# Kernel optimization log

Measured on AMD Instinct MI355X. Metric: run time of the kernel, lower is better.

The kernel has to match this reference:

```python
import jax, jax.numpy as jnp
import numpy as np

B, F, V, D = 16384, 26, 100000, 64
H1, H2 = 512, 256
IN_DIM = F * D + F * (F - 1) // 2  # 1664 + 325 = 1989
# upper-triangle (i<j) pair indices in row-major order == itertools.combinations order
IU, JU = np.triu_indices(F, k=1)


def setup_inputs() -> dict:
    key = jax.random.key(0)
    ks = jax.random.split(key, 9)
    idx = jax.random.randint(ks[0], (B, F), 0, V)
    tables = jax.random.normal(ks[1], (F, V, D), dtype=jnp.float32) * 0.01
    W1 = jax.random.normal(ks[2], (IN_DIM, H1), dtype=jnp.float32) * (IN_DIM ** -0.5)
    b1 = jnp.zeros((H1,), jnp.float32)
    W2 = jax.random.normal(ks[3], (H1, H2), dtype=jnp.float32) * (H1 ** -0.5)
    b2 = jnp.zeros((H2,), jnp.float32)
    W3 = jax.random.normal(ks[4], (H2, 1), dtype=jnp.float32) * (H2 ** -0.5)
    b3 = jnp.zeros((1,), jnp.float32)
    return {"idx": idx, "tables": tables, "W1": W1, "b1": b1,
            "W2": W2, "b2": b2, "W3": W3, "b3": b3}


def reference(idx, tables, W1, b1, W2, b2, W3, b3):
    # embedding lookup: tables[f, idx[b, f]] -> [B, F, D]
    emb = tables[jnp.arange(F)[None, :], idx]
    # fused dot-interaction: batched Gram matrix + triangular gather
    gram = jnp.einsum('bfd,bgd->bfg', emb, emb)  # [B, F, F]
    inter = gram[:, IU, JU]                      # [B, F*(F-1)/2]
    joint = jnp.concatenate([emb.reshape(B, F * D), inter], axis=1)
    h = jax.nn.relu(joint @ W1 + b1)
    h = jax.nn.relu(h @ W2 + b2)
    return (h @ W3 + b3).squeeze(-1)  # [B] logits
```

## Files before the change

### kernel.cpp

```cpp
#include <hip/hip_runtime.h>

#define B_SZ   16384
#define F_N    26
#define V_N    100000
#define D_N    64
#define H1_N   512
#define H2_N   256
#define IN_DIM 1989
#define KPAD   2048

typedef _Float16 half8_t __attribute__((ext_vector_type(8)));
typedef _Float16 half4_t __attribute__((ext_vector_type(4)));
typedef float    floatx4 __attribute__((ext_vector_type(4)));

#define MFMA16(a, b, c) __builtin_amdgcn_mfma_f32_16x16x32_f16((a), (b), (c), 0, 0, 0)

__device__ __forceinline__ void load_lds16(const void* g, void* l) {
    __builtin_amdgcn_global_load_lds(
        (const __attribute__((address_space(1))) unsigned int*)g,
        (__attribute__((address_space(3))) unsigned int*)l,
        16, 0, 0);
}

__global__ __launch_bounds__(256) void prep_w(const float* __restrict__ W,
                                              _Float16* __restrict__ WT,
                                              int K, int N, int Kpad) {
    int t = blockIdx.x * 256 + threadIdx.x;
    if (t >= N * Kpad) return;
    int n = t / Kpad;
    int k = t - n * Kpad;
    WT[t] = (k < K) ? (_Float16)W[(size_t)k * N + n] : (_Float16)0.f;
}

#define EMB_STRIDE 72
#define EMB_PER_SAMPLE (32 * EMB_STRIDE)

__global__ __launch_bounds__(256) void gather_interact(
        const int* __restrict__ idx,
        const float* __restrict__ tables,
        _Float16* __restrict__ joint) {
    __shared__ __align__(16) _Float16 embh[4 * EMB_PER_SAMPLE];
    __shared__ int sidx[4 * F_N];
    const int tid = threadIdx.x;
    const int b0  = blockIdx.x * 4;

    if (tid < 4 * F_N) sidx[tid] = idx[(size_t)b0 * F_N + tid];

    for (int z = tid; z < 4 * 6 * 16; z += 256) {
        int s = z / 96, rem = z % 96;
        int f = F_N + rem / 16, d4 = (rem % 16) * 4;
        half4_t zz; zz[0] = 0; zz[1] = 0; zz[2] = 0; zz[3] = 0;
        *(half4_t*)(embh + s * EMB_PER_SAMPLE + f * EMB_STRIDE + d4) = zz;
    }
    __syncthreads();

    for (int c = tid; c < 4 * F_N * 16; c += 256) {
        int s = c / 416, rem = c % 416;
        int f = rem >> 4, d4 = (rem & 15) * 4;
        const float4 v = *(const float4*)(tables +
                           ((size_t)f * V_N + sidx[s * F_N + f]) * D_N + d4);
        half4_t h;
        h[0] = (_Float16)v.x; h[1] = (_Float16)v.y;
        h[2] = (_Float16)v.z; h[3] = (_Float16)v.w;
        *(half4_t*)(embh + s * EMB_PER_SAMPLE + f * EMB_STRIDE + d4) = h;
        *(half4_t*)(joint + (size_t)(b0 + s) * KPAD + f * D_N + d4) = h;
    }
    for (int q = tid; q < 4 * (KPAD - IN_DIM); q += 256) {
        int s = q / (KPAD - IN_DIM), p = q % (KPAD - IN_DIM);
        joint[(size_t)(b0 + s) * KPAD + IN_DIM + p] = (_Float16)0.f;
    }
    __syncthreads();

    const int wave = tid >> 6, lane = tid & 63;
    const _Float16* eb = embh + wave * EMB_PER_SAMPLE;
    const int fr = lane & 15;
    const int fk = (lane >> 4) * 8;
    floatx4 a00 = {0.f, 0.f, 0.f, 0.f};
    floatx4 a01 = {0.f, 0.f, 0.f, 0.f};
    floatx4 a11 = {0.f, 0.f, 0.f, 0.f};
    #pragma unroll
    for (int k0 = 0; k0 < 64; k0 += 32) {
        half8_t f0 = *(const half8_t*)(eb + fr * EMB_STRIDE + k0 + fk);
        half8_t f1 = *(const half8_t*)(eb + (16 + fr) * EMB_STRIDE + k0 + fk);
        a00 = MFMA16(f0, f0, a00);
        a01 = MFMA16(f0, f1, a01);
        a11 = MFMA16(f1, f1, a11);
    }
    _Float16* jrow = joint + (size_t)(b0 + wave) * KPAD + F_N * D_N;
    #pragma unroll
    for (int r = 0; r < 4; ++r) {
        int mb = (lane >> 4) * 4 + r;
        {
            int m = mb, n = fr;
            if (m < n) jrow[(m * (51 - m)) / 2 + n - m - 1] = (_Float16)a00[r];
        }
        {
            int m = mb, n = 16 + fr;
            if (n < F_N) jrow[(m * (51 - m)) / 2 + n - m - 1] = (_Float16)a01[r];
        }
        {
            int m = 16 + mb, n = 16 + fr;
            if (m < n && n < F_N) jrow[(m * (51 - m)) / 2 + n - m - 1] = (_Float16)a11[r];
        }
    }
}

__global__ __launch_bounds__(256) void gemm_bt(
        const _Float16* __restrict__ A, int lda,
        const _Float16* __restrict__ Bt, int ldb,
        const float* __restrict__ bias,
        _Float16* __restrict__ C, int ldc,
        int K, int nblocks) {
    __shared__ __align__(16) _Float16 As[128 * 32];
    __shared__ __align__(16) _Float16 Bs[128 * 32];
    const int tid  = threadIdx.x;
    const int wave = tid >> 6;
    const int lane = tid & 63;
    const int bm = blockIdx.x / nblocks;
    const int bn = blockIdx.x % nblocks;
    const int m0 = bm * 128, n0 = bn * 128;

    const int c0 = tid, c1 = tid + 256;
    const _Float16* ag0 = A  + (size_t)(m0 + (c0 >> 2)) * lda + (c0 & 3) * 8;
    const _Float16* ag1 = A  + (size_t)(m0 + (c1 >> 2)) * lda + (c1 & 3) * 8;
    const _Float16* bg0 = Bt + (size_t)(n0 + (c0 >> 2)) * ldb + (c0 & 3) * 8;
    const _Float16* bg1 = Bt + (size_t)(n0 + (c1 >> 2)) * ldb + (c1 & 3) * 8;
    char* asd0 = (char*)As + wave * 1024;
    char* asd1 = (char*)As + 4096 + wave * 1024;
    char* bsd0 = (char*)Bs + wave * 1024;
    char* bsd1 = (char*)Bs + 4096 + wave * 1024;

    floatx4 acc[4][4];
    #pragma unroll
    for (int i = 0; i < 4; ++i)
        #pragma unroll
        for (int j = 0; j < 4; ++j) acc[i][j] = (floatx4){0.f, 0.f, 0.f, 0.f};

    const int wm = (wave >> 1) * 64;
    const int wn = (wave & 1) * 64;
    const int fr = lane & 15;
    const int fk = (lane >> 4) * 8;

    for (int k0 = 0; k0 < K; k0 += 32) {
        load_lds16(ag0 + k0, asd0);
        load_lds16(ag1 + k0, asd1);
        load_lds16(bg0 + k0, bsd0);
        load_lds16(bg1 + k0, bsd1);
        __syncthreads();
        half8_t af[4], bf[4];
        #pragma unroll
        for (int i = 0; i < 4; ++i)
            af[i] = *(const half8_t*)(As + (wm + i * 16 + fr) * 32 + fk);
        #pragma unroll
        for (int j = 0; j < 4; ++j)
            bf[j] = *(const half8_t*)(Bs + (wn + j * 16 + fr) * 32 + fk);
        #pragma unroll
        for (int i = 0; i < 4; ++i)
            #pragma unroll
            for (int j = 0; j < 4; ++j)
                acc[i][j] = MFMA16(af[i], bf[j], acc[i][j]);
        __syncthreads();
    }

    const int colb = n0 + wn + fr;
    const int rowb = m0 + wm + (lane >> 4) * 4;
    #pragma unroll
    for (int j = 0; j < 4; ++j) {
        const int c = colb + j * 16;
        const float bv = bias[c];
        #pragma unroll
        for (int i = 0; i < 4; ++i)
            #pragma unroll
            for (int r = 0; r < 4; ++r) {
                float v = acc[i][j][r] + bv;
                v = fmaxf(v, 0.f);
                C[(size_t)(rowb + i * 16 + r) * ldc + c] = (_Float16)v;
            }
    }
}

__global__ __launch_bounds__(256) void final_gemv(
        const _Float16* __restrict__ h2, const float* __restrict__ W3,
        const float* __restrict__ b3, float* __restrict__ out) {
    const int lane = threadIdx.x & 63;
    const int row  = blockIdx.x * 4 + (threadIdx.x >> 6);
    const float4 w = *(const float4*)(W3 + lane * 4);
    const half4_t h = *(const half4_t*)(h2 + (size_t)row * H2_N + lane * 4);
    float s = (float)h[0] * w.x + (float)h[1] * w.y +
              (float)h[2] * w.z + (float)h[3] * w.w;
    #pragma unroll
    for (int off = 32; off > 0; off >>= 1) s += __shfl_down(s, off, 64);
    if (lane == 0) out[row] = s + b3[0];
}

extern "C" void kernel_launch(void* const* d_in, const int* in_sizes, int n_in,
                              void* d_out, int out_size, void* d_ws, size_t ws_size,
                              hipStream_t stream) {
    const int*   idx    = (const int*)d_in[0];
    const float* tables = (const float*)d_in[1];
    const float* W1     = (const float*)d_in[2];
    const float* b1     = (const float*)d_in[3];
    const float* W2     = (const float*)d_in[4];
    const float* b2     = (const float*)d_in[5];
    const float* W3     = (const float*)d_in[6];
    const float* b3     = (const float*)d_in[7];
    float* out = (float*)d_out;

    char* ws = (char*)d_ws;
    _Float16* joint = (_Float16*)(ws);
    _Float16* W1T   = (_Float16*)(ws + 67108864);
    _Float16* h1    = (_Float16*)(ws + 69206016);
    _Float16* W2T   = (_Float16*)(ws + 85983232);
    _Float16* h2    = (_Float16*)(ws + 86245376);

    prep_w<<<(H1_N * KPAD + 255) / 256, 256, 0, stream>>>(W1, W1T, IN_DIM, H1_N, KPAD);
    prep_w<<<(H2_N * H1_N + 255) / 256, 256, 0, stream>>>(W2, W2T, H1_N, H2_N, H1_N);
    gather_interact<<<B_SZ / 4, 256, 0, stream>>>(idx, tables, joint);
    gemm_bt<<<(B_SZ / 128) * (H1_N / 128), 256, 0, stream>>>(
        joint, KPAD, W1T, KPAD, b1, h1, H1_N, KPAD, H1_N / 128);
    gemm_bt<<<(B_SZ / 128) * (H2_N / 128), 256, 0, stream>>>(
        h1, H1_N, W2T, H1_N, b2, h2, H2_N, H1_N, H2_N / 128);
    final_gemv<<<B_SZ / 4, 256, 0, stream>>>(h2, W3, b3, out);
}
```

Baseline: 835.7 us.

## Fuse second GEMM with final GEMV, swizzle GEMM blocks, batch gather loads

Replaces the second GEMM and the final GEMV with a single kernel that computes h1·W2, applies bias and ReLU, and reduces against W3 in registers and LDS, so h2 is never written or reread. The weight transpose kernel is remapped so it reads W coalesced, and GEMM block indices are remapped across XCDs for cache locality. The embedding gather issues all table loads before converting, to increase memory-level parallelism. The fused tail uses 512-thread blocks with fewer blocks in total, which may lower occupancy.

```diff
diff --git a/kernel.cpp b/kernel.cpp
--- a/kernel.cpp
+++ b/kernel.cpp
@@ -27,9 +27,9 @@
                                               int K, int N, int Kpad) {
     int t = blockIdx.x * 256 + threadIdx.x;
     if (t >= N * Kpad) return;
-    int n = t / Kpad;
-    int k = t - n * Kpad;
-    WT[t] = (k < K) ? (_Float16)W[(size_t)k * N + n] : (_Float16)0.f;
+    int k = t / N;
+    int n = t - k * N;
+    WT[(size_t)n * Kpad + k] = (k < K) ? (_Float16)W[(size_t)k * N + n] : (_Float16)0.f;
 }
 
 #define EMB_STRIDE 72
@@ -54,16 +54,29 @@
     }
     __syncthreads();
 
-    for (int c = tid; c < 4 * F_N * 16; c += 256) {
-        int s = c / 416, rem = c % 416;
-        int f = rem >> 4, d4 = (rem & 15) * 4;
-        const float4 v = *(const float4*)(tables +
-                           ((size_t)f * V_N + sidx[s * F_N + f]) * D_N + d4);
-        half4_t h;
-        h[0] = (_Float16)v.x; h[1] = (_Float16)v.y;
-        h[2] = (_Float16)v.z; h[3] = (_Float16)v.w;
-        *(half4_t*)(embh + s * EMB_PER_SAMPLE + f * EMB_STRIDE + d4) = h;
-        *(half4_t*)(joint + (size_t)(b0 + s) * KPAD + f * D_N + d4) = h;
+    float4 v[7];
+    #pragma unroll
+    for (int i = 0; i < 7; ++i) {
+        int c = tid + i * 256;
+        if (c < 4 * F_N * 16) {
+            int s = c / 416, rem = c - s * 416;
+            int f = rem >> 4, d4 = (rem & 15) * 4;
+            v[i] = *(const float4*)(tables +
+                     ((size_t)f * V_N + sidx[s * F_N + f]) * D_N + d4);
+        }
+    }
+    #pragma unroll
+    for (int i = 0; i < 7; ++i) {
+        int c = tid + i * 256;
+        if (c < 4 * F_N * 16) {
+            int s = c / 416, rem = c - s * 416;
+            int f = rem >> 4, d4 = (rem & 15) * 4;
+            half4_t h;
+            h[0] = (_Float16)v[i].x; h[1] = (_Float16)v[i].y;
+            h[2] = (_Float16)v[i].z; h[3] = (_Float16)v[i].w;
+            *(half4_t*)(embh + s * EMB_PER_SAMPLE + f * EMB_STRIDE + d4) = h;
+            *(half4_t*)(joint + (size_t)(b0 + s) * KPAD + f * D_N + d4) = h;
+        }
     }
     for (int q = tid; q < 4 * (KPAD - IN_DIM); q += 256) {
         int s = q / (KPAD - IN_DIM), p = q % (KPAD - IN_DIM);
@@ -116,8 +129,13 @@
     const int tid  = threadIdx.x;
     const int wave = tid >> 6;
     const int lane = tid & 63;
-    const int bm = blockIdx.x / nblocks;
-    const int bn = blockIdx.x % nblocks;
+    int bid = blockIdx.x;
+    if ((gridDim.x & 7) == 0) {
+        const int cpx = gridDim.x >> 3;
+        bid = (bid & 7) * cpx + (bid >> 3);
+    }
+    const int bm = bid / nblocks;
+    const int bn = bid % nblocks;
     const int m0 = bm * 128, n0 = bn * 128;
 
     const int c0 = tid, c1 = tid + 256;
@@ -179,18 +197,87 @@
     }
 }
 
-__global__ __launch_bounds__(256) void final_gemv(
-        const _Float16* __restrict__ h2, const float* __restrict__ W3,
+__global__ __launch_bounds__(512) void fused_tail(
+        const _Float16* __restrict__ h1, const _Float16* __restrict__ W2T,
+        const float* __restrict__ b2, const float* __restrict__ W3,
         const float* __restrict__ b3, float* __restrict__ out) {
-    const int lane = threadIdx.x & 63;
-    const int row  = blockIdx.x * 4 + (threadIdx.x >> 6);
-    const float4 w = *(const float4*)(W3 + lane * 4);
-    const half4_t h = *(const half4_t*)(h2 + (size_t)row * H2_N + lane * 4);
-    float s = (float)h[0] * w.x + (float)h[1] * w.y +
-              (float)h[2] * w.z + (float)h[3] * w.w;
-    #pragma unroll
-    for (int off = 32; off > 0; off >>= 1) s += __shfl_down(s, off, 64);
-    if (lane == 0) out[row] = s + b3[0];
+    __shared__ __align__(16) _Float16 As[128 * 32];
+    __shared__ __align__(16) _Float16 Bs[256 * 32];
+    __shared__ float red[4][128];
+    const int tid  = threadIdx.x;
+    const int wave = tid >> 6;
+    const int lane = tid & 63;
+    const int m0 = blockIdx.x * 128;
+
+    const int ca = tid, cb0 = tid, cb1 = tid + 512;
+    const _Float16* ag  = h1  + (size_t)(m0 + (ca >> 2)) * H1_N + (ca & 3) * 8;
+    const _Float16* bg0 = W2T + (size_t)(cb0 >> 2) * H1_N + (cb0 & 3) * 8;
+    const _Float16* bg1 = W2T + (size_t)(cb1 >> 2) * H1_N + (cb1 & 3) * 8;
+    char* asd  = (char*)As + wave * 1024;
+    char* bsd0 = (char*)Bs + wave * 1024;
+    char* bsd1 = (char*)Bs + 8192 + wave * 1024;
+
+    floatx4 acc[4][4];
+    #pragma unroll
+    for (int i = 0; i < 4; ++i)
+        #pragma unroll
+        for (int j = 0; j < 4; ++j) acc[i][j] = (floatx4){0.f, 0.f, 0.f, 0.f};
+
+    const int wm = (wave >> 2) * 64;
+    const int wn = (wave & 3) * 64;
+    const int fr = lane & 15;
+    const int fk = (lane >> 4) * 8;
+
+    for (int k0 = 0; k0 < H1_N; k0 += 32) {
+        load_lds16(ag  + k0, asd);
+        load_lds16(bg0 + k0, bsd0);
+        load_lds16(bg1 + k0, bsd1);
+        __syncthreads();
+        half8_t af[4], bf[4];
+        #pragma unroll
+        for (int i = 0; i < 4; ++i)
+            af[i] = *(const half8_t*)(As + (wm + i * 16 + fr) * 32 + fk);
+        #pragma unroll
+        for (int j = 0; j < 4; ++j)
+            bf[j] = *(const half8_t*)(Bs + (wn + j * 16 + fr) * 32 + fk);
+        #pragma unroll
+        for (int i = 0; i < 4; ++i)
+            #pragma unroll
+            for (int j = 0; j < 4; ++j)
+                acc[i][j] = MFMA16(af[i], bf[j], acc[i][j]);
+        __syncthreads();
+    }
+
+    float b2v[4], w3v[4];
+    #pragma unroll
+    for (int j = 0; j < 4; ++j) {
+        const int c = wn + j * 16 + fr;
+        b2v[j] = b2[c];
+        w3v[j] = W3[c];
+    }
+    #pragma unroll
+    for (int i = 0; i < 4; ++i)
+        #pragma unroll
+        for (int r = 0; r < 4; ++r) {
+            float p = 0.f;
+            #pragma unroll
+            for (int j = 0; j < 4; ++j) {
+                float h = acc[i][j][r] + b2v[j];
+                h = fmaxf(h, 0.f);
+                p += h * w3v[j];
+            }
+            p += __shfl_xor(p, 1, 16);
+            p += __shfl_xor(p, 2, 16);
+            p += __shfl_xor(p, 4, 16);
+            p += __shfl_xor(p, 8, 16);
+            if (fr == 0)
+                red[wave & 3][wm + i * 16 + (lane >> 4) * 4 + r] = p;
+        }
+    __syncthreads();
+    if (tid < 128) {
+        float s = red[0][tid] + red[1][tid] + red[2][tid] + red[3][tid] + b3[0];
+        out[m0 + tid] = s;
+    }
 }
 
 extern "C" void kernel_launch(void* const* d_in, const int* in_sizes, int n_in,
@@ -211,14 +298,11 @@
     _Float16* W1T   = (_Float16*)(ws + 67108864);
     _Float16* h1    = (_Float16*)(ws + 69206016);
     _Float16* W2T   = (_Float16*)(ws + 85983232);
-    _Float16* h2    = (_Float16*)(ws + 86245376);
 
     prep_w<<<(H1_N * KPAD + 255) / 256, 256, 0, stream>>>(W1, W1T, IN_DIM, H1_N, KPAD);
     prep_w<<<(H2_N * H1_N + 255) / 256, 256, 0, stream>>>(W2, W2T, H1_N, H2_N, H1_N);
     gather_interact<<<B_SZ / 4, 256, 0, stream>>>(idx, tables, joint);
     gemm_bt<<<(B_SZ / 128) * (H1_N / 128), 256, 0, stream>>>(
         joint, KPAD, W1T, KPAD, b1, h1, H1_N, KPAD, H1_N / 128);
-    gemm_bt<<<(B_SZ / 128) * (H2_N / 128), 256, 0, stream>>>(
-        h1, H1_N, W2T, H1_N, b2, h2, H2_N, H1_N, H2_N / 128);
-    final_gemv<<<B_SZ / 4, 256, 0, stream>>>(h2, W3, b3, out);
-}
+    fused_tail<<<B_SZ / 128, 512, 0, stream>>>(h1, W2T, b2, W3, b3, out);
+}
```

After: 829.4 us. No clear change (-0.8%).
